# Performance work log

Hardware: AMD Instinct MI355X
Metric: run time of the kernel (lower is better)

The kernel has to match this reference:

```python
import jax, jax.numpy as jnp
import numpy as np

B, NS, NC, D = 32, 1024, 1024, 256   # batch, sentence len, comment len, latent/embedding dim
K = 128                              # co-attention latent size (self.k)
CLIP_R = 2.0
EPS = 1e-5

def _norm(x):
    return jnp.sqrt(jnp.maximum(jnp.sum(x * x, -1, keepdims=True), 1e-15))

def artanh(x):
    x = jnp.clip(x, -1 + 1e-5, 1 - 1e-5)
    return 0.5 * (jnp.log1p(x) - jnp.log1p(-x))

# ---------- Poincare ball, c = 1 ----------
def p_logmap0(y):
    yn = _norm(y)
    return artanh(yn) * y / yn

def p_expmap0(u):
    un = _norm(u)
    return jnp.tanh(un) * u / un

def mobius_add(x, y):
    xy = jnp.sum(x * y, -1, keepdims=True)
    x2 = jnp.sum(x * x, -1, keepdims=True)
    y2 = jnp.sum(y * y, -1, keepdims=True)
    num = (1 + 2 * xy + y2) * x + (1 - x2) * y
    den = jnp.maximum(1 + 2 * xy + x2 * y2, 1e-15)
    return num / den

def mobius_matvec(m, x):
    # geoopt convention: result = 'x @ m^T' transported through the ball
    xn = _norm(x)
    mx = jnp.matmul(x, jnp.swapaxes(m, -1, -2))
    mxn = _norm(mx)
    return jnp.tanh(mxn / xn * artanh(xn)) * mx / mxn

# ---------- Lorentz hyperboloid, k = 1 ----------
def l_expmap0_space(v_space):
    # exp map at origin of a tangent vector with zero time component
    vn = _norm(v_space)
    return jnp.concatenate([jnp.cosh(vn), jnp.sinh(vn) * v_space / vn], -1)

def euclid_to_lorentz(x):
    xn = _norm(x) + EPS
    x = x * jnp.minimum(1.0, CLIP_R / xn)  # clip_r feature clipping
    return l_expmap0_space(x)              # F.pad time=0 then expmap0

def lorentz_linear(x, W, b):
    y = jnp.matmul(x, W.T) + b
    space = y[..., 1:]
    time = jnp.sqrt(jnp.sum(space * space, -1, keepdims=True) + 1.0)
    return jnp.concatenate([time, space], -1)

def lorentz_act(x):
    space = jax.nn.gelu(x[..., 1:], approximate=False)
    time = jnp.sqrt(jnp.sum(space * space, -1, keepdims=True) + 1.0)
    return jnp.concatenate([time, space], -1)

def lorentz_to_poincare(x):
    return x[..., 1:] / (x[..., :1] + 1.0)

def l_inner(u, v):
    return -u[..., :1] * v[..., :1] + jnp.sum(u[..., 1:] * v[..., 1:], -1, keepdims=True)

def centroid(x, w):
    avg = jnp.matmul(w, x)  # weighted Lorentz average, then renormalize to hyperboloid
    den = jnp.sqrt(jnp.maximum(jnp.abs(l_inner(avg, avg)), 1e-8))
    return avg / den

def l_logmap0_space(x):
    t = jnp.maximum(x[..., :1], 1 + 1e-7)
    return jnp.arccosh(t) * x[..., 1:] / _norm(x[..., 1:])

def lorentz_concat(x, y):
    z = jnp.concatenate([l_logmap0_space(x), l_logmap0_space(y)], -1)
    return l_expmap0_space(z)


def setup_inputs() -> dict:
    key = jax.random.key(0)
    ks = jax.random.split(key, 8)
    sentence = jax.random.normal(ks[0], (B, NS, D), jnp.float32)
    comment = jax.random.normal(ks[1], (B, NC, D), jnp.float32)
    comment = 0.9 * comment / (_norm(comment) + 1.0)  # valid Poincare-ball points
    w = lambda k, o, i: jax.random.normal(k, (o, i), jnp.float32) * 0.05
    return {
        'sentence_rep': sentence,
        'comment_rep': comment,
        'Wl_W': w(ks[2], D + 1, D + 1), 'Wl_b': jnp.zeros((D + 1,), jnp.float32),
        'Wc_W': w(ks[3], K + 1, D + 1), 'Wc_b': jnp.zeros((K + 1,), jnp.float32),
        'Ws_W': w(ks[4], K + 1, D + 1), 'Ws_b': jnp.zeros((K + 1,), jnp.float32),
        'whs': jax.random.uniform(ks[5], (1, K), jnp.float32),
        'whc': jax.random.uniform(ks[6], (1, K), jnp.float32),
    }


def reference(sentence_rep, comment_rep, Wl_W, Wl_b, Wc_W, Wc_b, Ws_W, Ws_b, whs, whc):
    T = lambda a: jnp.swapaxes(a, -1, -2)
    # Fourier mixing (real part, as torch .float() on complex)
    s = jnp.fft.fft2(sentence_rep).real.astype(jnp.float32)
    c = jnp.fft.fft2(p_logmap0(comment_rep)).real.astype(jnp.float32)
    Ls = euclid_to_lorentz(s)            # [B,NS,D+1]
    Lc = euclid_to_lorentz(c)            # [B,NC,D+1]
    L = lorentz_linear(Lc, Wl_W, Wl_b)   # [B,NC,D+1]
    L = lorentz_act(jnp.einsum('bnd,bmd->bnm', Ls, L))  # [B,NS,NC] affinity
    # Ws(sentence) and Wc(comment) in Poincare coords (computed once; original recomputes)
    Hs_a = lorentz_to_poincare(lorentz_linear(Ls, Ws_W, Ws_b))  # [B,NS,K]
    Hc_a = lorentz_to_poincare(lorentz_linear(Lc, Wc_W, Wc_b))  # [B,NC,K]
    Hs_b = mobius_matvec(T(Hc_a), L)          # [B,NS,K]
    Hs = mobius_add(Hs_a, Hs_b)
    Hs = p_expmap0(jax.nn.gelu(p_logmap0(Hs), approximate=False))
    Hc_b = mobius_matvec(T(Hs_a), T(L))       # [B,NC,K]
    Hc = mobius_add(T(Hc_a), T(Hc_b))         # [B,K,NC]
    Hc = p_expmap0(jax.nn.gelu(p_logmap0(Hc), approximate=False))
    As = jax.nn.softmax(T(mobius_matvec(whs, Hs)), axis=-1)     # [B,1,NS]
    Ac = jax.nn.softmax(T(mobius_matvec(whc, T(Hc))), axis=-1)  # [B,1,NC]
    co_s = centroid(Ls, As)                   # [B,1,D+1]
    co_c = centroid(Lc, Ac)                   # [B,1,D+1]
    co_sc = jnp.squeeze(lorentz_concat(co_s, co_c), axis=1)     # [B,2D+1]
    return co_sc, As, Ac
```

## Files before the change

kernel.cpp:

```cpp
#include <hip/hip_runtime.h>
#include <cstdint>
#include <math.h>

#define NBATCH 32
#define NSQ 1024
#define NCQ 1024
#define DDIM 256
#define DP 257
#define KQ 128
#define KPAD 288
#define NFOLD 640
#define KF2 640
#define MXSPLIT 4194304

typedef __attribute__((ext_vector_type(8))) short short8;
typedef __attribute__((ext_vector_type(4))) float floatx4;

__device__ __forceinline__ float bf2f(ushort u) { return __uint_as_float(((uint)u) << 16); }
__device__ __forceinline__ ushort f2bf(float f) {
    uint u = __float_as_uint(f);
    return (ushort)((u + 0x7FFFu + ((u >> 16) & 1u)) >> 16);
}
__device__ __forceinline__ void gload16(const void* g, void* l) {
    __builtin_amdgcn_global_load_lds(
        (const __attribute__((address_space(1))) void*)g,
        (__attribute__((address_space(3))) void*)l,
        16, 0, 0);
}
__device__ __forceinline__ float artanh_clip(float x) {
    x = fminf(fmaxf(x, -1.0f + 1e-5f), 1.0f - 1e-5f);
    return 0.5f * (log1pf(x) - log1pf(-x));
}
__device__ __forceinline__ float gelu_f(float x) {
    return 0.5f * x * (1.0f + erff(x * 0.70710678118654752440f));
}
__device__ __forceinline__ float waveRedSum(float v) {
#pragma unroll
    for (int o = 32; o > 0; o >>= 1) v += __shfl_down(v, o, 64);
    return __shfl(v, 0, 64);
}
__device__ __forceinline__ void waveRedSum3(float& a, float& b, float& c) {
#pragma unroll
    for (int o = 32; o > 0; o >>= 1) {
        a += __shfl_down(a, o, 64);
        b += __shfl_down(b, o, 64);
        c += __shfl_down(c, o, 64);
    }
    a = __shfl(a, 0, 64); b = __shfl(b, 0, 64); c = __shfl(c, 0, 64);
}
__device__ __forceinline__ void waveRedSum2(float& a, float& b) {
#pragma unroll
    for (int o = 32; o > 0; o >>= 1) {
        a += __shfl_down(a, o, 64);
        b += __shfl_down(b, o, 64);
    }
    a = __shfl(a, 0, 64); b = __shfl(b, 0, 64);
}
__device__ __forceinline__ float blockRedSum(float v, float* buf) {
    int lane = threadIdx.x & 63, wid = threadIdx.x >> 6;
#pragma unroll
    for (int o = 32; o > 0; o >>= 1) v += __shfl_down(v, o, 64);
    __syncthreads();
    if (lane == 0) buf[wid] = v;
    __syncthreads();
    int nw = blockDim.x >> 6;
    float s = buf[0];
    for (int i = 1; i < nw; i++) s += buf[i];
    return s;
}
__device__ __forceinline__ float blockRedMax(float v, float* buf) {
    int lane = threadIdx.x & 63, wid = threadIdx.x >> 6;
#pragma unroll
    for (int o = 32; o > 0; o >>= 1) v = fmaxf(v, __shfl_down(v, o, 64));
    __syncthreads();
    if (lane == 0) buf[wid] = v;
    __syncthreads();
    int nw = blockDim.x >> 6;
    float s = buf[0];
    for (int i = 1; i < nw; i++) s = fmaxf(s, buf[i]);
    return s;
}

template <bool A_NN, bool B_NN, bool OUT_BF16, bool BIAS, bool ATOMIC, int NSPLIT, bool DUAL>
__global__ __launch_bounds__(256) void mfma_gemm(
    const short* __restrict__ A, int lda, int64_t sA,
    const short* __restrict__ B, int ldb, int64_t sB,
    void* __restrict__ Cv, int ldc, int64_t sC,
    const float* __restrict__ bias, int M, int N, int K,
    const short* __restrict__ A1, const short* __restrict__ B1, int64_t cOff1,
    const float* __restrict__ biasB)
{
    __shared__ short As[128][32];
    __shared__ short Bs[128][32];
    const int zz = blockIdx.z;
    int zb, ks, half;
    if (DUAL) { half = zz & 1; zb = zz >> 1; ks = 0; }
    else      { zb = zz / NSPLIT; ks = zz - zb * NSPLIT; half = 0; }
    const short* Ap = (DUAL && half) ? A1 : A;
    const short* Bp = (DUAL && half) ? B1 : B;
    Ap += (int64_t)zb * sA;
    Bp += (int64_t)zb * sB;
    const int kper = K / NSPLIT;
    const int kbeg = ks * kper, kend = kbeg + kper;
    const int m0 = blockIdx.y * 128, n0 = blockIdx.x * 128;
    const int t = threadIdx.x;
    const int lane = t & 63, w = t >> 6;
    const int wm = (w & 1) * 64, wn = (w >> 1) * 64;
    floatx4 acc[4][4] = {};
    for (int k0 = kbeg; k0 < kend; k0 += 32) {
        if (!A_NN) {
            int r = t >> 2, c8 = (t & 3) * 8;
            const short* ap = Ap + (int64_t)(m0 + r) * lda + k0 + c8;
            gload16(ap, &As[r][c8]);
            gload16(ap + (int64_t)64 * lda, &As[r + 64][c8]);
        } else {
            int r2 = t >> 4, c8 = (t & 15) * 8;
            int kk = 2 * r2;
            const ushort* a0 = (const ushort*)Ap + (int64_t)(k0 + kk) * lda + m0 + c8;
            uint4 v0 = *(const uint4*)a0;
            uint4 v1 = *(const uint4*)(a0 + lda);
            const ushort* p0 = (const ushort*)&v0;
            const ushort* p1 = (const ushort*)&v1;
#pragma unroll
            for (int i = 0; i < 8; i++) {
                uint pk = (uint)p0[i] | ((uint)p1[i] << 16);
                *(uint*)&As[c8 + i][kk] = pk;
            }
        }
        if (!B_NN) {
            int r = t >> 2, c8 = (t & 3) * 8;
            const short* bp = Bp + (int64_t)(n0 + r) * ldb + k0 + c8;
            gload16(bp, &Bs[r][c8]);
            gload16(bp + (int64_t)64 * ldb, &Bs[r + 64][c8]);
        } else {
            int r2 = t >> 4, c8 = (t & 15) * 8;
            int kk = 2 * r2;
            const ushort* b0 = (const ushort*)Bp + (int64_t)(k0 + kk) * ldb + n0 + c8;
            uint4 v0 = *(const uint4*)b0;
            uint4 v1 = *(const uint4*)(b0 + ldb);
            const ushort* p0 = (const ushort*)&v0;
            const ushort* p1 = (const ushort*)&v1;
#pragma unroll
            for (int i = 0; i < 8; i++) {
                uint pk = (uint)p0[i] | ((uint)p1[i] << 16);
                *(uint*)&Bs[c8 + i][kk] = pk;
            }
        }
        __syncthreads();
        short8 af[4], bfv[4];
#pragma unroll
        for (int i = 0; i < 4; i++)
            af[i] = *(const short8*)&As[wm + 16 * i + (lane & 15)][8 * (lane >> 4)];
#pragma unroll
        for (int i = 0; i < 4; i++)
            bfv[i] = *(const short8*)&Bs[wn + 16 * i + (lane & 15)][8 * (lane >> 4)];
#pragma unroll
        for (int i = 0; i < 4; i++)
#pragma unroll
            for (int j = 0; j < 4; j++)
                acc[i][j] = __builtin_amdgcn_mfma_f32_16x16x32_bf16(af[i], bfv[j], acc[i][j], 0, 0, 0);
        __syncthreads();
    }
    const int q = lane >> 4, c = lane & 15;
    int64_t cbase = (int64_t)zb * sC + ((DUAL && half) ? cOff1 : 0);
    if (NSPLIT > 1 && !ATOMIC) cbase += (int64_t)ks * cOff1;
    const float* bsel = (BIAS && biasB && zb) ? biasB : bias;
#pragma unroll
    for (int j = 0; j < 4; j++) {
        int col = n0 + wn + 16 * j + c;
        float bv = BIAS ? bsel[col] : 0.0f;
#pragma unroll
        for (int i = 0; i < 4; i++) {
            int rowb = m0 + wm + 16 * i + 4 * q;
#pragma unroll
            for (int r = 0; r < 4; r++) {
                float v = acc[i][j][r] + bv;
                int64_t idx = cbase + (int64_t)(rowb + r) * ldc + col;
                if (ATOMIC)       atomicAdd((float*)Cv + idx, v);
                else if (OUT_BF16) ((ushort*)Cv)[idx] = f2bf(v);
                else               ((float*)Cv)[idx] = v;
            }
        }
    }
}

__global__ __launch_bounds__(256) void genconst_kernel(
    ushort* CS1c, ushort* CS1s, ushort* C2, ushort* S2,
    const float* __restrict__ WlW, const float* __restrict__ WsW, const float* __restrict__ WcW,
    ushort* Wl, ushort* Ws, ushort* Wc)
{
    int blk = blockIdx.x, t = threadIdx.x;
    if (blk < 3200) {
        int idx = blk * 256 + t;
        int hs = idx >= 409600;
        int e = idx - hs * 409600;
        int n = e / KF2, k = e - n * KF2;
        float v = 0.0f;
        if (k <= 512) {
            int p = (n * k) & 1023;
            float ang = (6.28318530717958647692f / 1024.0f) * (float)p;
            v = hs ? ((k == 0) ? 0.0f : -sinf(ang)) : cosf(ang);
        }
        (hs ? CS1s : CS1c)[e] = f2bf(v);
    } else if (blk < 3456) {
        int idx = (blk - 3200) * 256 + t;
        int d = idx >> 8, j = idx & 255;
        int p = (d * j) & 255;
        float ang = (6.28318530717958647692f / 256.0f) * (float)p;
        C2[idx] = f2bf(cosf(ang));
        S2[idx] = f2bf(sinf(ang));
    } else {
        int r = blk - 3456;
        const float* src; ushort* dst; int srow;
        if (r < 256)      { src = WlW; dst = Wl + r * KPAD;        srow = r + 1; }
        else if (r < 384) { src = WsW; dst = Ws + (r - 256) * KPAD; srow = r - 256 + 1; }
        else              { src = WcW; dst = Wc + (r - 384) * KPAD; srow = r - 384 + 1; }
        dst[t] = (t < DP) ? f2bf(src[(int64_t)srow * DP + t]) : (ushort)0;
        if (t < KPAD - 256) {
            int t2 = t + 256;
            dst[t2] = (t2 < DP) ? f2bf(src[(int64_t)srow * DP + t2]) : (ushort)0;
        }
    }
}

__global__ __launch_bounds__(256) void prep_fold_kernel(const float* __restrict__ sent,
                                                        const float* __restrict__ comm,
                                                        ushort* __restrict__ XC, ushort* __restrict__ XS) {
    int bp = blockIdx.x;
    int z = blockIdx.y * 4 + (threadIdx.x >> 6);
    int lane = threadIdx.x & 63;
    int m2 = (1024 - bp) & 1023;
    const float* base = (z < 32) ? sent + (int64_t)z * 262144 : comm + (int64_t)(z - 32) * 262144;
    float4 a = *(const float4*)(base + bp * 256 + 4 * lane);
    float4 b = *(const float4*)(base + m2 * 256 + 4 * lane);
    if (z >= 32) {
        float s1 = a.x * a.x + a.y * a.y + a.z * a.z + a.w * a.w;
        float s2 = b.x * b.x + b.y * b.y + b.z * b.z + b.w * b.w;
        waveRedSum2(s1, s2);
        float yn1 = sqrtf(fmaxf(s1, 1e-15f));
        float f1 = artanh_clip(yn1) / yn1;
        a.x *= f1; a.y *= f1; a.z *= f1; a.w *= f1;
        float yn2 = sqrtf(fmaxf(s2, 1e-15f));
        float f2v = artanh_clip(yn2) / yn2;
        b.x *= f2v; b.y *= f2v; b.z *= f2v; b.w *= f2v;
    }
    int64_t o = ((int64_t)z * NFOLD + bp) * 256 + 4 * lane;
    bool single = (bp == 0) || (bp == 512);
    ushort4 oc;
    oc.x = f2bf(single ? a.x : a.x + b.x);
    oc.y = f2bf(single ? a.y : a.y + b.y);
    oc.z = f2bf(single ? a.z : a.z + b.z);
    oc.w = f2bf(single ? a.w : a.w + b.w);
    *(ushort4*)(XC + o) = oc;
    if (!single) {
        ushort4 os;
        os.x = f2bf(a.x - b.x); os.y = f2bf(a.y - b.y);
        os.z = f2bf(a.z - b.z); os.w = f2bf(a.w - b.w);
        *(ushort4*)(XS + o) = os;
    }
}

__global__ __launch_bounds__(256) void e2l_kernel(const ushort* __restrict__ YcYs,
                                                  ushort* __restrict__ Lsb, ushort* __restrict__ Lcb) {
    int64_t row = (int64_t)blockIdx.x * 4 + (threadIdx.x >> 6);
    int lane = threadIdx.x & 63;
    int z = (int)(row >> 10), n = (int)(row & 1023);
    int np = (n <= 512) ? n : 1024 - n;
    float sgn = (n <= 512) ? 1.0f : -1.0f;
    const ushort* base = YcYs + (int64_t)z * 327680 + np * 256 + 4 * lane;
    ushort4 uc = *(const ushort4*)base;
    ushort4 us = *(const ushort4*)(base + 163840);
    float v0 = bf2f(uc.x) + sgn * bf2f(us.x);
    float v1 = bf2f(uc.y) + sgn * bf2f(us.y);
    float v2 = bf2f(uc.z) + sgn * bf2f(us.z);
    float v3 = bf2f(uc.w) + sgn * bf2f(us.w);
    float s = waveRedSum(v0 * v0 + v1 * v1 + v2 * v2 + v3 * v3);
    float xn = sqrtf(fmaxf(s, 1e-15f)) + 1e-5f;
    float sc = fminf(1.0f, 2.0f / xn);
    float s2 = fmaxf(s * sc * sc, 1e-15f);
    float vn = sqrtf(s2);
    float e = expf(vn);
    float ei = 1.0f / e;
    float shv = (vn < 1e-4f) ? 1.0f : (e - ei) * 0.5f / vn;
    float fac = shv * sc;
    ushort* ob = (row < 32768 ? Lsb + row * KPAD : Lcb + (row - 32768) * KPAD);
    ob[1 + 4 * lane + 0] = f2bf(fac * v0);
    ob[1 + 4 * lane + 1] = f2bf(fac * v1);
    ob[1 + 4 * lane + 2] = f2bf(fac * v2);
    ob[1 + 4 * lane + 3] = f2bf(fac * v3);
    if (lane == 0) ob[0] = f2bf((e + ei) * 0.5f);
    if (lane < KPAD - DP) ob[DP + lane] = 0;
}

__global__ __launch_bounds__(256) void lnorm_kernel(ushort* __restrict__ Llin_bf) {
    int64_t row = (int64_t)blockIdx.x * 4 + (threadIdx.x >> 6);
    int lane = threadIdx.x & 63;
    ushort* ob = Llin_bf + row * KPAD;
    float s = 0.f;
#pragma unroll
    for (int i = 0; i < 4; i++) { float v = bf2f(ob[1 + 4 * lane + i]); s += v * v; }
    s = waveRedSum(s);
    if (lane == 0) ob[0] = f2bf(sqrtf(s + 1.0f));
    if (lane < KPAD - DP) ob[DP + lane] = 0;
}

__global__ __launch_bounds__(256) void poinc2_kernel(ushort* __restrict__ Hcat) {
    int64_t row = (int64_t)blockIdx.x * 4 + (threadIdx.x >> 6);
    int lane = threadIdx.x & 63;
    ushort* r = Hcat + row * KQ;
    ushort2 u = *(ushort2*)&r[2 * lane];
    float v0 = bf2f(u.x), v1 = bf2f(u.y);
    float s = waveRedSum(v0 * v0 + v1 * v1);
    float inv = 1.0f / (sqrtf(s + 1.0f) + 1.0f);
    ushort2 o; o.x = f2bf(v0 * inv); o.y = f2bf(v1 * inv);
    *(ushort2*)&r[2 * lane] = o;
}

__global__ __launch_bounds__(256) void lact_kernel(ushort* __restrict__ Lmat, float* __restrict__ xnrow) {
    __shared__ float red[4];
    int64_t row = blockIdx.x; int t = threadIdx.x;
    ushort* r = Lmat + row * (int64_t)NCQ;
    ushort4 u = *(ushort4*)&r[4 * t];
    float v[4] = {bf2f(u.x), bf2f(u.y), bf2f(u.z), bf2f(u.w)};
    float g[4]; float s = 0.f;
#pragma unroll
    for (int i = 0; i < 4; i++) {
        int idx = 4 * t + i;
        if (idx > 0) { g[i] = gelu_f(v[i]); s += g[i] * g[i]; } else g[i] = 0.f;
    }
    s = blockRedSum(s, red);
    if (t == 0) g[0] = sqrtf(1.0f + s);
    ushort4 o; o.x = f2bf(g[0]); o.y = f2bf(g[1]); o.z = f2bf(g[2]); o.w = f2bf(g[3]);
    *(ushort4*)&r[4 * t] = o;
    if (t == 0) xnrow[row] = sqrtf(fmaxf(1.0f + 2.0f * s, 1e-15f));
}

__global__ void tmat_kernel(const ushort* __restrict__ in, ushort* __restrict__ outp) {
    __shared__ ushort tile[32][33];
    int z = blockIdx.z;
    int r0 = blockIdx.x * 32, c0 = blockIdx.y * 32;
    const ushort* ib = in + (int64_t)z * 1048576;
    ushort* ob = outp + (int64_t)z * 1048576;
    int tx = threadIdx.x, ty = threadIdx.y;
    for (int i = 0; i < 32; i += 8) tile[ty + i][tx] = ib[(r0 + ty + i) * 1024 + c0 + tx];
    __syncthreads();
    for (int i = 0; i < 32; i += 8) ob[(c0 + ty + i) * 1024 + r0 + tx] = tile[tx][ty + i];
}

__global__ __launch_bounds__(256) void colnormA_kernel(const ushort* __restrict__ Lmat, float* __restrict__ part) {
    int b = blockIdx.x, chunk = blockIdx.y, t = threadIdx.x;
    const ushort* base = Lmat + (int64_t)b * NSQ * NCQ + (int64_t)chunk * 128 * NCQ + 4 * t;
    float s0 = 0.f, s1 = 0.f, s2 = 0.f, s3 = 0.f;
    for (int n = 0; n < 128; n++) {
        ushort4 u = *(const ushort4*)(base + (int64_t)n * NCQ);
        float a = bf2f(u.x), bb = bf2f(u.y), c = bf2f(u.z), d = bf2f(u.w);
        s0 += a * a; s1 += bb * bb; s2 += c * c; s3 += d * d;
    }
    float4 o = {s0, s1, s2, s3};
    *(float4*)(part + ((int64_t)(b * 8 + chunk)) * 4096 + 4 * t) = o;
}
__global__ __launch_bounds__(256) void colfac_kernel(const float* __restrict__ part,
                                                     const float* __restrict__ mxcT,
                                                     float* __restrict__ fac_c) {
    int b = blockIdx.x; int m = blockIdx.y * 256 + threadIdx.x;
    const float* p = part + (int64_t)b * 8 * 4096 + m;
    float s = 0.f;
#pragma unroll
    for (int c = 0; c < 8; c++) s += p[c * 4096];
    float xn = sqrtf(fmaxf(s, 1e-15f));
    const float* base = mxcT + (int64_t)b * KQ * NCQ + m;
    const float* base2 = base + MXSPLIT;
    float sm = 0.f;
    for (int j = 0; j < KQ; j++) {
        float v = base[j * NCQ] + base2[j * NCQ];
        sm += v * v;
    }
    float mxn = sqrtf(fmaxf(sm, 1e-15f));
    fac_c[b * NCQ + m] = tanhf(mxn / xn * artanh_clip(xn)) / mxn;
}

__global__ __launch_bounds__(256) void rowops_s_kernel(
    const ushort* __restrict__ Hsa, const float* __restrict__ mxs,
    const float* __restrict__ xnrow, const float* __restrict__ whs,
    float* __restrict__ logits)
{
    const int t = threadIdx.x;
    const int lane = t & 63;
    const int wid = t >> 6;
    const int sub = lane & 7;
    const int rg  = lane >> 3;
    const int64_t row = (int64_t)blockIdx.x * 32 + wid * 8 + rg;
    const ushort* p = Hsa + row * KQ + sub * 16;
    const float*  q = mxs + row * KQ + sub * 16;

    float pf[16], qf[16];
    {
        uint4 u0 = *(const uint4*)p;
        uint4 u1 = *(const uint4*)(p + 8);
        const ushort* pu0 = (const ushort*)&u0;
        const ushort* pu1 = (const ushort*)&u1;
#pragma unroll
        for (int i = 0; i < 8; i++) { pf[i] = bf2f(pu0[i]); pf[8 + i] = bf2f(pu1[i]); }
    }
#pragma unroll
    for (int i = 0; i < 16; i += 4) {
        float4 a  = *(const float4*)(q + i);
        float4 b2 = *(const float4*)(q + i + MXSPLIT);
        qf[i + 0] = a.x + b2.x; qf[i + 1] = a.y + b2.y;
        qf[i + 2] = a.z + b2.z; qf[i + 3] = a.w + b2.w;
    }
    float r1 = 0.f, r2 = 0.f, r3 = 0.f;
#pragma unroll
    for (int i = 0; i < 16; i++) {
        r1 += qf[i] * qf[i]; r2 += pf[i] * qf[i]; r3 += pf[i] * pf[i];
    }
#pragma unroll
    for (int o = 4; o > 0; o >>= 1) {
        r1 += __shfl_xor(r1, o, 64);
        r2 += __shfl_xor(r2, o, 64);
        r3 += __shfl_xor(r3, o, 64);
    }
    float mxn = sqrtf(fmaxf(r1, 1e-15f));
    float xn = xnrow[row];
    float fac = tanhf(mxn / xn * artanh_clip(xn)) / mxn;
    float xy = fac * r2;
    float x2 = r3;
    float y2 = fac * fac * r1;
    float ca = 1.f + 2.f * xy + y2, cb = 1.f - x2;
    float den = fmaxf(1.f + 2.f * xy + x2 * y2, 1e-15f);
    float hn2 = (ca * ca * x2 + 2.f * ca * cb * xy + cb * cb * y2) / (den * den);
    float hn = sqrtf(fmaxf(hn2, 1e-15f));
    float uf = artanh_clip(hn) / hn;
    float ufd = uf / den;
    float cbf = cb * fac;
    float wv[16];
#pragma unroll
    for (int i = 0; i < 16; i += 4) *(float4*)&wv[i] = *(const float4*)(whs + sub * 16 + i);
    float r4 = 0.f, r5 = 0.f;
#pragma unroll
    for (int i = 0; i < 16; i++) {
        float g = gelu_f(ufd * (ca * pf[i] + cbf * qf[i]));
        r4 += g * g;
        r5 += g * wv[i];
    }
#pragma unroll
    for (int o = 4; o > 0; o >>= 1) {
        r4 += __shfl_xor(r4, o, 64);
        r5 += __shfl_xor(r5, o, 64);
    }
    float gn = sqrtf(fmaxf(r4, 1e-15f));
    float ef = tanhf(gn) / gn;
    float dot = ef * r5;
    float Hn = sqrtf(fmaxf(ef * ef * r4, 1e-15f));
    float mxn2 = sqrtf(fmaxf(dot * dot, 1e-15f));
    float lg = tanhf(mxn2 / Hn * artanh_clip(Hn)) * dot / mxn2;
    if (sub == 0) logits[row] = lg;
}

__global__ void thsa_kernel(const ushort* __restrict__ in, ushort* __restrict__ outp) {
    __shared__ ushort tile[32][33];
    int z = blockIdx.z;
    int n0 = blockIdx.x * 32, j0 = blockIdx.y * 32;
    const ushort* ib = in + (int64_t)z * 131072;
    ushort* ob = outp + (int64_t)z * 131072;
    int tx = threadIdx.x, ty = threadIdx.y;
    for (int i = 0; i < 32; i += 8) tile[ty + i][tx] = ib[(n0 + ty + i) * 128 + j0 + tx];
    __syncthreads();
    for (int i = 0; i < 32; i += 8) ob[(j0 + ty + i) * 1024 + n0 + tx] = tile[tx][ty + i];
}

__global__ __launch_bounds__(256) void rowops_c_kernel(const ushort* __restrict__ HcAT,
                                                       float* __restrict__ mx,
                                                       const float* __restrict__ fac_c) {
    int64_t row = (int64_t)blockIdx.x * 4 + (threadIdx.x >> 6);
    int lane = threadIdx.x & 63;
    int b = (int)(row >> 7);
    const ushort* xb = HcAT + row * (int64_t)NCQ + 16 * lane;
    float* yb = mx + row * (int64_t)NCQ + 16 * lane;
    const float* fb = fac_c + b * NCQ + 16 * lane;
    float xv[16], yv[16];
    {
        uint4 u0 = *(const uint4*)xb;
        uint4 u1 = *(const uint4*)(xb + 8);
        const ushort* pu0 = (const ushort*)&u0;
        const ushort* pu1 = (const ushort*)&u1;
#pragma unroll
        for (int i = 0; i < 8; i++) { xv[i] = bf2f(pu0[i]); xv[8 + i] = bf2f(pu1[i]); }
    }
#pragma unroll
    for (int i = 0; i < 16; i += 4) {
        float4 v1 = *(const float4*)(yb + i);
        float4 v2 = *(const float4*)(yb + i + MXSPLIT);
        float4 fv = *(const float4*)(fb + i);
        yv[i + 0] = fv.x * (v1.x + v2.x);
        yv[i + 1] = fv.y * (v1.y + v2.y);
        yv[i + 2] = fv.z * (v1.z + v2.z);
        yv[i + 3] = fv.w * (v1.w + v2.w);
    }
    float xy = 0.f, x2 = 0.f, y2 = 0.f;
#pragma unroll
    for (int i = 0; i < 16; i++) { xy += xv[i] * yv[i]; x2 += xv[i] * xv[i]; y2 += yv[i] * yv[i]; }
    waveRedSum3(xy, x2, y2);
    float ca = 1.f + 2.f * xy + y2, cb = 1.f - x2;
    float den = fmaxf(1.f + 2.f * xy + x2 * y2, 1e-15f);
    float hn2 = (ca * ca * x2 + 2.f * ca * cb * xy + cb * cb * y2) / (den * den);
    float hn = sqrtf(fmaxf(hn2, 1e-15f));
    float uf = artanh_clip(hn) / hn;
    float g[16]; float gn2 = 0.f;
#pragma unroll
    for (int i = 0; i < 16; i++) {
        float h = (ca * xv[i] + cb * yv[i]) / den;
        g[i] = gelu_f(uf * h);
        gn2 += g[i] * g[i];
    }
    gn2 = waveRedSum(gn2);
    float gn = sqrtf(fmaxf(gn2, 1e-15f));
    float ef = tanhf(gn) / gn;
#pragma unroll
    for (int i = 0; i < 16; i += 4) {
        float4 o = {ef * g[i], ef * g[i + 1], ef * g[i + 2], ef * g[i + 3]};
        *(float4*)(yb + i) = o;
    }
}

__global__ __launch_bounds__(256) void logitsc_kernel(const float* __restrict__ Hc, const float* __restrict__ whc, float* __restrict__ lgc) {
    int b = blockIdx.x; int m = blockIdx.y * 256 + threadIdx.x;
    const float* base = Hc + (int64_t)b * KQ * NCQ + m;
    float s1 = 0.f, s2 = 0.f;
    for (int j = 0; j < KQ; j++) { float v = base[j * NCQ]; s1 += v * whc[j]; s2 += v * v; }
    float xn = sqrtf(fmaxf(s2, 1e-15f));
    float mxn = sqrtf(fmaxf(s1 * s1, 1e-15f));
    lgc[b * NCQ + m] = tanhf(mxn / xn * artanh_clip(xn)) * s1 / mxn;
}

__global__ __launch_bounds__(256) void softmax_kernel(const float* __restrict__ lg, float* __restrict__ outp) {
    __shared__ float red[4];
    int b = blockIdx.x; int t = threadIdx.x;
    const float* x = lg + b * 1024;
    float v[4]; float m = -1e30f;
#pragma unroll
    for (int i = 0; i < 4; i++) { v[i] = x[t + 256 * i]; m = fmaxf(m, v[i]); }
    m = blockRedMax(m, red);
    float s = 0.f;
#pragma unroll
    for (int i = 0; i < 4; i++) { v[i] = expf(v[i] - m); s += v[i]; }
    s = blockRedSum(s, red);
    float inv = 1.0f / s;
#pragma unroll
    for (int i = 0; i < 4; i++) outp[b * 1024 + t + 256 * i] = v[i] * inv;
}

__global__ __launch_bounds__(320) void centroidA_kernel(
    const ushort* __restrict__ Lsb, const ushort* __restrict__ Lcb,
    const float* __restrict__ As, const float* __restrict__ Ac,
    float* __restrict__ part)
{
    int b = blockIdx.x;
    int which = blockIdx.y;
    int chunk = blockIdx.z;
    const ushort* L = which ? Lcb : Lsb;
    const float* w = which ? Ac : As;
    int t = threadIdx.x;
    if (t >= DP) return;
    const ushort* Lb = L + (int64_t)b * NSQ * KPAD + (int64_t)chunk * 128 * KPAD + t;
    const float* wb = w + b * NSQ + chunk * 128;
    float s = 0.f;
    for (int n = 0; n < 128; n++) s += wb[n] * bf2f(Lb[(int64_t)n * KPAD]);
    part[((int64_t)((b * 2 + which) * 8 + chunk)) * 264 + t] = s;
}
__global__ __launch_bounds__(320) void centroidB_kernel(
    const float* __restrict__ part, float* __restrict__ co_s, float* __restrict__ co_c)
{
    int b = blockIdx.x;
    int which = blockIdx.y;
    int t = threadIdx.x;
    if (t >= DP) return;
    const float* p = part + (int64_t)(b * 2 + which) * 8 * 264 + t;
    float s = 0.f;
#pragma unroll
    for (int c = 0; c < 8; c++) s += p[c * 264];
    (which ? co_c : co_s)[b * DP + t] = s;
}

__global__ __launch_bounds__(256) void final_kernel(const float* __restrict__ co_s, const float* __restrict__ co_c, float* __restrict__ outp) {
    __shared__ float red[4];
    int b = blockIdx.x, t = threadIdx.x;
    float zmine[2];
    for (int w = 0; w < 2; w++) {
        const float* co = (w ? co_c : co_s) + b * DP;
        float at = co[0];
        float asp = co[1 + t];
        float ssp = blockRedSum(asp * asp, red);
        float li = ssp - at * at;
        float den = sqrtf(fmaxf(fabsf(li), 1e-8f));
        float xt = at / den, xsp = asp / den;
        float s2 = blockRedSum(xsp * xsp, red);
        float nrm = sqrtf(fmaxf(s2, 1e-15f));
        float ac = acoshf(fmaxf(xt, 1.0f + 1e-7f));
        zmine[w] = ac * xsp / nrm;
    }
    float vn2 = blockRedSum(zmine[0] * zmine[0] + zmine[1] * zmine[1], red);
    float vn = sqrtf(fmaxf(vn2, 1e-15f));
    float sc = sinhf(vn) / vn;
    if (t == 0) outp[b * 513] = coshf(vn);
    outp[b * 513 + 1 + t] = sc * zmine[0];
    outp[b * 513 + 1 + 256 + t] = sc * zmine[1];
}

extern "C" void kernel_launch(void* const* d_in, const int* in_sizes, int n_in,
                              void* d_out, int out_size, void* d_ws, size_t ws_size,
                              hipStream_t stream)
{
    const float* sent = (const float*)d_in[0];
    const float* comm = (const float*)d_in[1];
    const float* WlW  = (const float*)d_in[2];
    const float* Wlb  = (const float*)d_in[3];
    const float* WcW  = (const float*)d_in[4];
    const float* Wcb  = (const float*)d_in[5];
    const float* WsW  = (const float*)d_in[6];
    const float* Wsb  = (const float*)d_in[7];
    const float* whs  = (const float*)d_in[8];
    const float* whc  = (const float*)d_in[9];
    float* out = (float*)d_out;
    (void)in_sizes; (void)n_in; (void)out_size; (void)ws_size;

    float* ws = (float*)d_ws;
    size_t off = 0;
    auto take = [&](size_t n) { float* p = ws + off; off += n; return p; };
    float*  xnrow = take(32768);
    float*  fac_c = take(32768);
    float*  lgs   = take(32768);
    float*  lgc   = take(32768);
    float*  co_s  = take(8224);
    float*  co_c  = take(8224);
    ushort* Ls_bf = (ushort*)take(4718592);
    ushort* Lc_bf = (ushort*)take(4718592);
    ushort* Wl_bf = (ushort*)take(36864);
    ushort* Ws_bf = (ushort*)take(18432);
    ushort* Wc_bf = (ushort*)take(18432);
    ushort* HsA_bf = (ushort*)take(2097152);
    ushort* HcA_bf = (ushort*)take(2097152);
    float*  part_cn   = take(1048576);
    float*  part_cent = take(135168);
    ushort* LmatT_bf  = (ushort*)take(16777216);
    float*  F     = take(33554432);

    ushort* XC_bf   = (ushort*)F;
    ushort* XS_bf   = (ushort*)(F + 5242880);
    ushort* Ff_bf   = (ushort*)(F + 10485760);
    ushort* CS1c    = (ushort*)(F + 20971520);
    ushort* CS1s    = (ushort*)(F + 21176320);
    ushort* C2_bf   = (ushort*)(F + 21381120);
    ushort* S2_bf   = (ushort*)(F + 21413888);
    ushort* YcYs    = (ushort*)F;
    ushort* Lmat_bf = (ushort*)F;
    ushort* Llin_bf = (ushort*)(F + 29360128);
    float*  mx      = F + 16777216;
    ushort* HsAT    = (ushort*)(F + 25165824);
    ushort* HcAT    = (ushort*)(F + 27262976);

    float* AsOut = out + 16416;
    float* AcOut = out + 16416 + 32768;

    dim3 blk(256);
    const short* NUL = nullptr;

    genconst_kernel<<<3968, 256, 0, stream>>>(CS1c, CS1s, C2_bf, S2_bf, WlW, WsW, WcW, Wl_bf, Ws_bf, Wc_bf);

    prep_fold_kernel<<<dim3(513, 16), blk, 0, stream>>>(sent, comm, XC_bf, XS_bf);
    mfma_gemm<false,false,true,false,false,1,true><<<dim3(5,2,128), blk, 0, stream>>>(
        (const short*)C2_bf,256,0, (const short*)XC_bf,256,(int64_t)NFOLD*256, Ff_bf,1280,(int64_t)256*1280,
        nullptr, 256,NFOLD,256, (const short*)S2_bf, (const short*)XS_bf, 640, nullptr);
    mfma_gemm<false,false,true,false,false,1,true><<<dim3(2,5,128), blk, 0, stream>>>(
        (const short*)CS1c,KF2,0, (const short*)Ff_bf,1280,(int64_t)256*1280, YcYs,256,327680,
        nullptr, NFOLD,256,KF2, (const short*)CS1s, (const short*)(Ff_bf+640), 163840, nullptr);
    e2l_kernel<<<16384, blk, 0, stream>>>(YcYs, Ls_bf, Lc_bf);

    mfma_gemm<false,false,true,true,false,1,false><<<dim3(2,256,1), blk, 0, stream>>>(
        (const short*)Lc_bf,KPAD,0, (const short*)Wl_bf,KPAD,0, (void*)(Llin_bf+1),KPAD,0,
        Wlb+1, 32768,256,KPAD, NUL, NUL, 0, nullptr);
    lnorm_kernel<<<8192, blk, 0, stream>>>(Llin_bf);

    mfma_gemm<false,false,true,false,false,1,false><<<dim3(8,8,32), blk, 0, stream>>>(
        (const short*)Ls_bf,KPAD,294912, (const short*)Llin_bf,KPAD,294912, Lmat_bf,1024,1048576,
        nullptr, 1024,1024,KPAD, NUL, NUL, 0, nullptr);
    lact_kernel<<<32768, blk, 0, stream>>>(Lmat_bf, xnrow);
    tmat_kernel<<<dim3(32,32,32), dim3(32,8), 0, stream>>>(Lmat_bf, LmatT_bf);
    colnormA_kernel<<<dim3(32,8), blk, 0, stream>>>(Lmat_bf, part_cn);

    mfma_gemm<false,false,true,true,false,1,false><<<dim3(1,256,2), blk, 0, stream>>>(
        (const short*)Ls_bf,KPAD,9437184, (const short*)Ws_bf,KPAD,36864, HsA_bf,128,4194304,
        Wsb+1, 32768,128,KPAD, NUL, NUL, 0, Wcb+1);
    poinc2_kernel<<<16384, blk, 0, stream>>>(HsA_bf);

    thsa_kernel<<<dim3(32,4,64), dim3(32,8), 0, stream>>>(HsA_bf, HsAT);

    mfma_gemm<false,false,false,false,false,2,false><<<dim3(1,8,64), blk, 0, stream>>>(
        (const short*)Lmat_bf,1024,1048576, (const short*)HcAT,1024,131072, mx,128,131072,
        nullptr, 1024,128,1024, NUL, NUL, MXSPLIT, nullptr);
    rowops_s_kernel<<<1024, blk, 0, stream>>>(HsA_bf, mx, xnrow, whs, lgs);

    mfma_gemm<false,false,false,false,false,2,false><<<dim3(8,1,64), blk, 0, stream>>>(
        (const short*)HsAT,1024,131072, (const short*)LmatT_bf,1024,1048576, mx,1024,131072,
        nullptr, 128,1024,1024, NUL, NUL, MXSPLIT, nullptr);
    colfac_kernel<<<dim3(32,4), blk, 0, stream>>>(part_cn, mx, fac_c);
    rowops_c_kernel<<<1024, blk, 0, stream>>>(HcAT, mx, fac_c);
    logitsc_kernel<<<dim3(32,4), blk, 0, stream>>>(mx, whc, lgc);

    softmax_kernel<<<64, blk, 0, stream>>>(lgs, AsOut);
    centroidA_kernel<<<dim3(32,2,8), 320, 0, stream>>>(Ls_bf, Lc_bf, AsOut, AcOut, part_cent);
    centroidB_kernel<<<dim3(32,2), 320, 0, stream>>>(part_cent, co_s, co_c);
    final_kernel<<<32, blk, 0, stream>>>(co_s, co_c, out);
}
```

Measured before the change: 514.8 us.

## Fuse GELU into affinity GEMM epilogue and fold norm reductions into transpose

```diff
diff --git a/kernel.cpp b/kernel.cpp
--- a/kernel.cpp
+++ b/kernel.cpp
@@ -81,7 +81,7 @@
     return s;
 }
 
-template <bool A_NN, bool B_NN, bool OUT_BF16, bool BIAS, bool ATOMIC, int NSPLIT, bool DUAL>
+template <bool A_NN, bool B_NN, bool OUT_BF16, bool BIAS, bool ATOMIC, int NSPLIT, bool DUAL, bool GELU = false>
 __global__ __launch_bounds__(256) void mfma_gemm(
     const short* __restrict__ A, int lda, int64_t sA,
     const short* __restrict__ B, int ldb, int64_t sB,
@@ -175,6 +175,7 @@
 #pragma unroll
             for (int r = 0; r < 4; r++) {
                 float v = acc[i][j][r] + bv;
+                if (GELU) v = gelu_f(v);
                 int64_t idx = cbase + (int64_t)(rowb + r) * ldc + col;
                 if (ATOMIC)       atomicAdd((float*)Cv + idx, v);
                 else if (OUT_BF16) ((ushort*)Cv)[idx] = f2bf(v);
@@ -316,26 +317,8 @@
     *(ushort2*)&r[2 * lane] = o;
 }
 
-__global__ __launch_bounds__(256) void lact_kernel(ushort* __restrict__ Lmat, float* __restrict__ xnrow) {
-    __shared__ float red[4];
-    int64_t row = blockIdx.x; int t = threadIdx.x;
-    ushort* r = Lmat + row * (int64_t)NCQ;
-    ushort4 u = *(ushort4*)&r[4 * t];
-    float v[4] = {bf2f(u.x), bf2f(u.y), bf2f(u.z), bf2f(u.w)};
-    float g[4]; float s = 0.f;
-#pragma unroll
-    for (int i = 0; i < 4; i++) {
-        int idx = 4 * t + i;
-        if (idx > 0) { g[i] = gelu_f(v[i]); s += g[i] * g[i]; } else g[i] = 0.f;
-    }
-    s = blockRedSum(s, red);
-    if (t == 0) g[0] = sqrtf(1.0f + s);
-    ushort4 o; o.x = f2bf(g[0]); o.y = f2bf(g[1]); o.z = f2bf(g[2]); o.w = f2bf(g[3]);
-    *(ushort4*)&r[4 * t] = o;
-    if (t == 0) xnrow[row] = sqrtf(fmaxf(1.0f + 2.0f * s, 1e-15f));
-}
-
-__global__ void tmat_kernel(const ushort* __restrict__ in, ushort* __restrict__ outp) {
+__global__ void tmat_kernel(const ushort* __restrict__ in, ushort* __restrict__ outp,
+                            float* __restrict__ rowpart, float* __restrict__ colpart) {
     __shared__ ushort tile[32][33];
     int z = blockIdx.z;
     int r0 = blockIdx.x * 32, c0 = blockIdx.y * 32;
@@ -345,29 +328,60 @@
     for (int i = 0; i < 32; i += 8) tile[ty + i][tx] = ib[(r0 + ty + i) * 1024 + c0 + tx];
     __syncthreads();
     for (int i = 0; i < 32; i += 8) ob[(c0 + ty + i) * 1024 + r0 + tx] = tile[tx][ty + i];
-}
-
-__global__ __launch_bounds__(256) void colnormA_kernel(const ushort* __restrict__ Lmat, float* __restrict__ part) {
-    int b = blockIdx.x, chunk = blockIdx.y, t = threadIdx.x;
-    const ushort* base = Lmat + (int64_t)b * NSQ * NCQ + (int64_t)chunk * 128 * NCQ + 4 * t;
-    float s0 = 0.f, s1 = 0.f, s2 = 0.f, s3 = 0.f;
-    for (int n = 0; n < 128; n++) {
-        ushort4 u = *(const ushort4*)(base + (int64_t)n * NCQ);
-        float a = bf2f(u.x), bb = bf2f(u.y), c = bf2f(u.z), d = bf2f(u.w);
-        s0 += a * a; s1 += bb * bb; s2 += c * c; s3 += d * d;
-    }
-    float4 o = {s0, s1, s2, s3};
-    *(float4*)(part + ((int64_t)(b * 8 + chunk)) * 4096 + 4 * t) = o;
-}
-__global__ __launch_bounds__(256) void colfac_kernel(const float* __restrict__ part,
+    int id = ty * 32 + tx;
+    if (id < 32) {
+        float s = 0.f;
+        for (int r = 0; r < 32; r++) { float v = bf2f(tile[r][id]); s += v * v; }
+        colpart[((int64_t)(z * 32 + blockIdx.x)) * 1024 + c0 + id] = s;
+    } else if (id < 64) {
+        int rid = id - 32;
+        float s = 0.f;
+        int cstart = (c0 == 0) ? 1 : 0;
+        for (int c = cstart; c < 32; c++) { float v = bf2f(tile[rid][c]); s += v * v; }
+        rowpart[((int64_t)(z * 32 + blockIdx.y)) * 1024 + r0 + rid] = s;
+    }
+}
+
+__global__ __launch_bounds__(256) void combine_kernel(
+    const float* __restrict__ rowpart, const float* __restrict__ colpart,
+    ushort* __restrict__ Lmat, ushort* __restrict__ LmatT,
+    float* __restrict__ xnrow, float* __restrict__ colsum)
+{
+    __shared__ float red[4];
+    int b = blockIdx.x, t = threadIdx.x;
+    float t2 = 0.f;
+#pragma unroll
+    for (int i = 0; i < 4; i++) {
+        int n = t + 256 * i;
+        const float* rp = rowpart + (int64_t)b * 32768 + n;
+        float s = 0.f;
+#pragma unroll
+        for (int c = 0; c < 32; c++) s += rp[c * 1024];
+        float tim = sqrtf(1.0f + s);
+        ushort tb = f2bf(tim);
+        Lmat[((int64_t)(b * 1024 + n)) * 1024] = tb;
+        LmatT[(int64_t)b * 1048576 + n] = tb;
+        xnrow[b * 1024 + n] = sqrtf(fmaxf(1.0f + 2.0f * s, 1e-15f));
+        t2 += tim * tim;
+    }
+#pragma unroll
+    for (int i = 0; i < 4; i++) {
+        int m = t + 256 * i;
+        const float* cp = colpart + (int64_t)b * 32768 + m;
+        float s = 0.f;
+#pragma unroll
+        for (int c = 0; c < 32; c++) s += cp[c * 1024];
+        if (m > 0) colsum[b * 1024 + m] = s;
+    }
+    float tt = blockRedSum(t2, red);
+    if (t == 0) colsum[b * 1024] = tt;
+}
+
+__global__ __launch_bounds__(256) void colfac_kernel(const float* __restrict__ colsum,
                                                      const float* __restrict__ mxcT,
                                                      float* __restrict__ fac_c) {
     int b = blockIdx.x; int m = blockIdx.y * 256 + threadIdx.x;
-    const float* p = part + (int64_t)b * 8 * 4096 + m;
-    float s = 0.f;
-#pragma unroll
-    for (int c = 0; c < 8; c++) s += p[c * 4096];
-    float xn = sqrtf(fmaxf(s, 1e-15f));
+    float xn = sqrtf(fmaxf(colsum[b * NCQ + m], 1e-15f));
     const float* base = mxcT + (int64_t)b * KQ * NCQ + m;
     const float* base2 = base + MXSPLIT;
     float sm = 0.f;
@@ -658,6 +672,8 @@
     float*  mx      = F + 16777216;
     ushort* HsAT    = (ushort*)(F + 25165824);
     ushort* HcAT    = (ushort*)(F + 27262976);
+    float*  colpart = F + 29360128;
+    float*  colsum  = F + 30408704;
 
     float* AsOut = out + 16416;
     float* AcOut = out + 16416 + 32768;
@@ -681,12 +697,11 @@
         Wlb+1, 32768,256,KPAD, NUL, NUL, 0, nullptr);
     lnorm_kernel<<<8192, blk, 0, stream>>>(Llin_bf);
 
-    mfma_gemm<false,false,true,false,false,1,false><<<dim3(8,8,32), blk, 0, stream>>>(
+    mfma_gemm<false,false,true,false,false,1,false,true><<<dim3(8,8,32), blk, 0, stream>>>(
         (const short*)Ls_bf,KPAD,294912, (const short*)Llin_bf,KPAD,294912, Lmat_bf,1024,1048576,
         nullptr, 1024,1024,KPAD, NUL, NUL, 0, nullptr);
-    lact_kernel<<<32768, blk, 0, stream>>>(Lmat_bf, xnrow);
-    tmat_kernel<<<dim3(32,32,32), dim3(32,8), 0, stream>>>(Lmat_bf, LmatT_bf);
-    colnormA_kernel<<<dim3(32,8), blk, 0, stream>>>(Lmat_bf, part_cn);
+    tmat_kernel<<<dim3(32,32,32), dim3(32,8), 0, stream>>>(Lmat_bf, LmatT_bf, part_cn, colpart);
+    combine_kernel<<<32, blk, 0, stream>>>(part_cn, colpart, Lmat_bf, LmatT_bf, xnrow, colsum);
 
     mfma_gemm<false,false,true,true,false,1,false><<<dim3(1,256,2), blk, 0, stream>>>(
         (const short*)Ls_bf,KPAD,9437184, (const short*)Ws_bf,KPAD,36864, HsA_bf,128,4194304,
@@ -703,7 +718,7 @@
     mfma_gemm<false,false,false,false,false,2,false><<<dim3(8,1,64), blk, 0, stream>>>(
         (const short*)HsAT,1024,131072, (const short*)LmatT_bf,1024,1048576, mx,1024,131072,
         nullptr, 128,1024,1024, NUL, NUL, MXSPLIT, nullptr);
-    colfac_kernel<<<dim3(32,4), blk, 0, stream>>>(part_cn, mx, fac_c);
+    colfac_kernel<<<dim3(32,4), blk, 0, stream>>>(colsum, mx, fac_c);
     rowops_c_kernel<<<1024, blk, 0, stream>>>(HcAT, mx, fac_c);
     logitsc_kernel<<<dim3(32,4), blk, 0, stream>>>(mx, whc, lgc);
 
```

After: 516.0 us. About the same (+0.2%).
